# Optimization experiments

Measured on AMD Instinct MI355X. Metric: run time of the kernel, lower is better.

The kernel has to match this reference:

```python
import jax, jax.numpy as jnp
import numpy as np

TOP_K = 8
NUM_EXPERTS = 64
ALPHA = 0.01  # load_balance_alpha
TEMPERATURE = 1.0  # buffer value at init; eval mode so never decayed


def setup_inputs() -> dict:
    key = jax.random.key(0)
    k1, k2 = jax.random.split(key)
    x = jax.random.normal(k1, (4, 4096, 4096), dtype=jnp.float32)
    W_gate = jax.random.normal(k2, (64, 4096), dtype=jnp.float32) * (1.0 / np.sqrt(4096.0))
    return {"x": x, "W_gate": W_gate}


def reference(x, W_gate):
    B, S, H = x.shape
    x_flat = x.reshape(-1, H)                       # [N, H], N = B*S
    N = x_flat.shape[0]
    logits = jnp.einsum('nh,eh->ne', x_flat, W_gate)  # gate linear, bias=False
    logits = logits / TEMPERATURE                   # eval: no noise added
    scores, idx = jax.lax.top_k(logits, TOP_K)      # [N, K] values / indices
    # scatter mask -> per-expert usage counts (equivalent to scatter_(1, idx, 1).sum(0))
    current_usage = jnp.zeros((NUM_EXPERTS,), dtype=x.dtype).at[idx.reshape(-1)].add(1.0)
    expert_load = current_usage / N
    ideal_load = 1.0 / NUM_EXPERTS
    load_balance_loss = ALPHA * jnp.sum((expert_load - ideal_load) ** 2)
    scores = jax.nn.softmax(scores.astype(jnp.float32), axis=-1).astype(x.dtype)
    return scores, idx, load_balance_loss
```

## Files before the change

kernel.cpp:

```cpp
#include <hip/hip_runtime.h>
#include <math.h>

#define NTOK 16384
#define HDIM 4096
#define NEXP 64
#define SPLITS 4
#define KRANGE (HDIM / SPLITS)
#define KC 32
#define TOKTILE 128
#define XSTRIDE (TOKTILE + 4)
#define WSTRIDE (NEXP + 4)

__global__ __launch_bounds__(512, 4) void gemm_tile(const float* __restrict__ x,
                                                    const float* __restrict__ W,
                                                    float* __restrict__ partial) {
  __shared__ __align__(16) float xs[KC][XSTRIDE];
  __shared__ __align__(16) float ws[KC][WSTRIDE];
  const int tile = (int)blockIdx.x >> 2;
  const int split = (int)blockIdx.x & 3;
  const int kbase = split * KRANGE;
  const int tok0 = tile * TOKTILE;
  const int t = (int)threadIdx.x;
  const int eg = t & 15;
  const int tg = t >> 4;

  const int srow = t >> 3;
  const int sc4 = (t & 7) * 4;
  const float* xsrc0 = x + (size_t)(tok0 + srow) * HDIM + kbase + sc4;
  const float* xsrc1 = x + (size_t)(tok0 + 64 + srow) * HDIM + kbase + sc4;
  const float* wsrc = W + (size_t)srow * HDIM + kbase + sc4;

  float4 xa0 = *(const float4*)xsrc0;
  float4 xa1 = *(const float4*)xsrc1;
  float4 wa = *(const float4*)wsrc;

  double acc[4][4];
#pragma unroll
  for (int i = 0; i < 4; ++i)
#pragma unroll
    for (int j = 0; j < 4; ++j) acc[i][j] = 0.0;

  for (int c = 0; c < KRANGE / KC; ++c) {
#pragma unroll
    for (int j = 0; j < 4; ++j) {
      xs[sc4 + j][srow] = ((const float*)&xa0)[j];
      xs[sc4 + j][64 + srow] = ((const float*)&xa1)[j];
      ws[sc4 + j][srow] = ((const float*)&wa)[j];
    }
    __syncthreads();
    if (c + 1 < KRANGE / KC) {
      xa0 = *(const float4*)(xsrc0 + (c + 1) * KC);
      xa1 = *(const float4*)(xsrc1 + (c + 1) * KC);
      wa = *(const float4*)(wsrc + (c + 1) * KC);
    }
    float p[4][4];
#pragma unroll
    for (int i = 0; i < 4; ++i)
#pragma unroll
      for (int j = 0; j < 4; ++j) p[i][j] = 0.0f;

#pragma unroll 8
    for (int k = 0; k < KC; ++k) {
      float4 xv = *(const float4*)&xs[k][4 * tg];
      float4 wv = *(const float4*)&ws[k][4 * eg];
#pragma unroll
      for (int i = 0; i < 4; ++i) {
        float xi = ((const float*)&xv)[i];
        p[i][0] = fmaf(xi, wv.x, p[i][0]);
        p[i][1] = fmaf(xi, wv.y, p[i][1]);
        p[i][2] = fmaf(xi, wv.z, p[i][2]);
        p[i][3] = fmaf(xi, wv.w, p[i][3]);
      }
    }
#pragma unroll
    for (int i = 0; i < 4; ++i)
#pragma unroll
      for (int j = 0; j < 4; ++j) acc[i][j] += (double)p[i][j];
    __syncthreads();
  }

#pragma unroll
  for (int j = 0; j < 4; ++j) {
    float4 o;
    o.x = (float)acc[0][j]; o.y = (float)acc[1][j];
    o.z = (float)acc[2][j]; o.w = (float)acc[3][j];
    *(float4*)&partial[((size_t)split * NEXP + 4 * eg + j) * NTOK + tok0 + 4 * tg] = o;
  }
}

__global__ __launch_bounds__(128) void topk_kernel(const float* __restrict__ partial,
                                                   float* __restrict__ out_scores,
                                                   float* __restrict__ out_idx,
                                                   unsigned int* __restrict__ counts) {
  const int n = blockIdx.x * 128 + threadIdx.x;
  __shared__ unsigned int lcnt[64];
  if (threadIdx.x < 64) lcnt[threadIdx.x] = 0u;
  __syncthreads();

  float v[8];
  int id[8];
#pragma unroll
  for (int j = 0; j < 8; ++j) { v[j] = -INFINITY; id[j] = 0; }

  for (int e = 0; e < 64; ++e) {
    double s = 0.0;
#pragma unroll
    for (int sp = 0; sp < SPLITS; ++sp)
      s += (double)partial[((size_t)sp * NEXP + e) * NTOK + n];
    float val = (float)s;
#pragma unroll
    for (int j = 7; j >= 0; --j) {
      if (val > v[j]) {
        if (j == 0 || val <= v[j - 1]) { v[j] = val; id[j] = e; }
        else { v[j] = v[j - 1]; id[j] = id[j - 1]; }
      }
    }
  }

  float ex[8], s = 0.0f;
#pragma unroll
  for (int j = 0; j < 8; ++j) { ex[j] = expf(v[j] - v[0]); s += ex[j]; }
  float inv = 1.0f / s;

#pragma unroll
  for (int j = 0; j < 8; ++j) {
    out_scores[(size_t)n * 8 + j] = ex[j] * inv;
    out_idx[(size_t)n * 8 + j] = (float)id[j];
    atomicAdd(&lcnt[id[j]], 1u);
  }
  __syncthreads();
  if (threadIdx.x < 64) atomicAdd(&counts[threadIdx.x], lcnt[threadIdx.x]);
}

__global__ __launch_bounds__(64) void loss_kernel(const unsigned int* __restrict__ counts,
                                                  float* __restrict__ out_loss) {
  const int e = threadIdx.x;
  double d = (double)counts[e] / (double)NTOK - 1.0 / 64.0;
  double sq = d * d;
#pragma unroll
  for (int off = 32; off > 0; off >>= 1) sq += __shfl_down(sq, off);
  if (e == 0) *out_loss = (float)(0.01 * sq);
}

extern "C" void kernel_launch(void* const* d_in, const int* in_sizes, int n_in,
                              void* d_out, int out_size, void* d_ws, size_t ws_size,
                              hipStream_t stream) {
  const float* x = (const float*)d_in[0];
  const float* W = (const float*)d_in[1];

  float* out = (float*)d_out;
  float* scores = out;
  float* idxf = out + (size_t)NTOK * 8;
  float* loss = out + (size_t)NTOK * 16;

  unsigned int* counts = (unsigned int*)d_ws;
  float* partial = (float*)((char*)d_ws + 256);

  hipMemsetAsync(d_ws, 0, 256, stream);
  gemm_tile<<<(NTOK / TOKTILE) * SPLITS, 512, 0, stream>>>(x, W, partial);
  topk_kernel<<<NTOK / 128, 128, 0, stream>>>(partial, scores, idxf, counts);
  loss_kernel<<<1, 64, 0, stream>>>(counts, loss);
}
```

Baseline: 453.3 us.

## Retile gating GEMM with 8x8 register blocking, swizzled LDS, wave-parallel top-k

Reworks the gating GEMM to 256-token tiles with 8 K-splits and an 8x8 fp32 register tile per thread. It replaces the transposed padded LDS layout with an XOR-swizzled float4 layout and drops the double-precision per-chunk accumulation. The partial logits are now stored token-major, so top-k can give each token one wavefront: each lane holds one expert and the 8 maxima are found by shuffle reductions. The aim is more FMA work per LDS read and less fp64 conversion cost, at the price of slightly different rounding from pure fp32 accumulation and more workspace traffic for the 8 splits.

```diff
diff --git a/kernel.cpp b/kernel.cpp
--- a/kernel.cpp
+++ b/kernel.cpp
@@ -4,137 +4,168 @@
 #define NTOK 16384
 #define HDIM 4096
 #define NEXP 64
-#define SPLITS 4
+#define SPLITS 8
 #define KRANGE (HDIM / SPLITS)
 #define KC 32
-#define TOKTILE 128
-#define XSTRIDE (TOKTILE + 4)
-#define WSTRIDE (NEXP + 4)
+#define NCHUNK (KRANGE / KC)
+#define TOKTILE 256
 
-__global__ __launch_bounds__(512, 4) void gemm_tile(const float* __restrict__ x,
+#define XGRAN 2048
+#define WGRAN 512
+#define BUFGRAN (XGRAN + WGRAN)
+
+__global__ __launch_bounds__(256, 2) void gemm_tile(const float* __restrict__ x,
                                                     const float* __restrict__ W,
                                                     float* __restrict__ partial) {
-  __shared__ __align__(16) float xs[KC][XSTRIDE];
-  __shared__ __align__(16) float ws[KC][WSTRIDE];
-  const int tile = (int)blockIdx.x >> 2;
-  const int split = (int)blockIdx.x & 3;
+  __shared__ __align__(16) float4 lds4[BUFGRAN];
+  const int bid = (int)blockIdx.x;
+  const int tile = bid >> 3;
+  const int split = bid & 7;
+  const int tok0 = tile * TOKTILE;
   const int kbase = split * KRANGE;
-  const int tok0 = tile * TOKTILE;
   const int t = (int)threadIdx.x;
-  const int eg = t & 15;
-  const int tg = t >> 4;
+  const int tg = t >> 3;
+  const int eg = t & 7;
 
   const int srow = t >> 3;
-  const int sc4 = (t & 7) * 4;
-  const float* xsrc0 = x + (size_t)(tok0 + srow) * HDIM + kbase + sc4;
-  const float* xsrc1 = x + (size_t)(tok0 + 64 + srow) * HDIM + kbase + sc4;
-  const float* wsrc = W + (size_t)srow * HDIM + kbase + sc4;
+  const int scg = t & 7;
+  const float* xsrc[8];
+  int xdst[8];
+#pragma unroll
+  for (int s = 0; s < 8; ++s) {
+    const int row = s * 32 + srow;
+    xsrc[s] = x + (size_t)(tok0 + row) * HDIM + kbase + scg * 4;
+    xdst[s] = row * 8 + (scg ^ ((row >> 3) & 7));
+  }
+  const float* wsrc[2];
+  int wdst[2];
+#pragma unroll
+  for (int s = 0; s < 2; ++s) {
+    const int row = s * 32 + srow;
+    wsrc[s] = W + (size_t)row * HDIM + kbase + scg * 4;
+    wdst[s] = XGRAN + row * 8 + (scg ^ ((row >> 3) & 7));
+  }
 
-  float4 xa0 = *(const float4*)xsrc0;
-  float4 xa1 = *(const float4*)xsrc1;
-  float4 wa = *(const float4*)wsrc;
+  float acc[8][8];
+#pragma unroll
+  for (int i = 0; i < 8; ++i)
+#pragma unroll
+    for (int j = 0; j < 8; ++j) acc[i][j] = 0.0f;
 
-  double acc[4][4];
+  float4 xa[8], wa[2];
 #pragma unroll
-  for (int i = 0; i < 4; ++i)
+  for (int s = 0; s < 8; ++s) xa[s] = *(const float4*)xsrc[s];
 #pragma unroll
-    for (int j = 0; j < 4; ++j) acc[i][j] = 0.0;
+  for (int s = 0; s < 2; ++s) wa[s] = *(const float4*)wsrc[s];
 
-  for (int c = 0; c < KRANGE / KC; ++c) {
+  const float4* xs4 = lds4 + tg * 64;
+  const float4* ws4 = lds4 + XGRAN + eg * 64;
+  const int xsw = tg & 7;
+
+#pragma unroll 1
+  for (int c = 0; c < NCHUNK; ++c) {
+    __syncthreads();
 #pragma unroll
-    for (int j = 0; j < 4; ++j) {
-      xs[sc4 + j][srow] = ((const float*)&xa0)[j];
-      xs[sc4 + j][64 + srow] = ((const float*)&xa1)[j];
-      ws[sc4 + j][srow] = ((const float*)&wa)[j];
+    for (int s = 0; s < 8; ++s) lds4[xdst[s]] = xa[s];
+#pragma unroll
+    for (int s = 0; s < 2; ++s) lds4[wdst[s]] = wa[s];
+    __syncthreads();
+
+    if (c + 1 < NCHUNK) {
+#pragma unroll
+      for (int s = 0; s < 8; ++s) xa[s] = *(const float4*)(xsrc[s] + (c + 1) * KC);
+#pragma unroll
+      for (int s = 0; s < 2; ++s) wa[s] = *(const float4*)(wsrc[s] + (c + 1) * KC);
     }
-    __syncthreads();
-    if (c + 1 < KRANGE / KC) {
-      xa0 = *(const float4*)(xsrc0 + (c + 1) * KC);
-      xa1 = *(const float4*)(xsrc1 + (c + 1) * KC);
-      wa = *(const float4*)(wsrc + (c + 1) * KC);
+
+#pragma unroll
+    for (int k4 = 0; k4 < 8; ++k4) {
+      float4 xf[8], wf[8];
+#pragma unroll
+      for (int i = 0; i < 8; ++i) xf[i] = xs4[i * 8 + (k4 ^ xsw)];
+#pragma unroll
+      for (int j = 0; j < 8; ++j) wf[j] = ws4[j * 8 + (k4 ^ eg)];
+#pragma unroll
+      for (int i = 0; i < 8; ++i)
+#pragma unroll
+        for (int j = 0; j < 8; ++j) {
+          acc[i][j] = fmaf(xf[i].x, wf[j].x, acc[i][j]);
+          acc[i][j] = fmaf(xf[i].y, wf[j].y, acc[i][j]);
+          acc[i][j] = fmaf(xf[i].z, wf[j].z, acc[i][j]);
+          acc[i][j] = fmaf(xf[i].w, wf[j].w, acc[i][j]);
+        }
     }
-    float p[4][4];
-#pragma unroll
-    for (int i = 0; i < 4; ++i)
-#pragma unroll
-      for (int j = 0; j < 4; ++j) p[i][j] = 0.0f;
-
-#pragma unroll 8
-    for (int k = 0; k < KC; ++k) {
-      float4 xv = *(const float4*)&xs[k][4 * tg];
-      float4 wv = *(const float4*)&ws[k][4 * eg];
-#pragma unroll
-      for (int i = 0; i < 4; ++i) {
-        float xi = ((const float*)&xv)[i];
-        p[i][0] = fmaf(xi, wv.x, p[i][0]);
-        p[i][1] = fmaf(xi, wv.y, p[i][1]);
-        p[i][2] = fmaf(xi, wv.z, p[i][2]);
-        p[i][3] = fmaf(xi, wv.w, p[i][3]);
-      }
-    }
-#pragma unroll
-    for (int i = 0; i < 4; ++i)
-#pragma unroll
-      for (int j = 0; j < 4; ++j) acc[i][j] += (double)p[i][j];
-    __syncthreads();
   }
 
 #pragma unroll
-  for (int j = 0; j < 4; ++j) {
-    float4 o;
-    o.x = (float)acc[0][j]; o.y = (float)acc[1][j];
-    o.z = (float)acc[2][j]; o.w = (float)acc[3][j];
-    *(float4*)&partial[((size_t)split * NEXP + 4 * eg + j) * NTOK + tok0 + 4 * tg] = o;
+  for (int i = 0; i < 8; ++i) {
+    const int tok = tok0 + tg * 8 + i;
+    float* dst = partial + ((size_t)split * NTOK + tok) * NEXP + eg * 8;
+    float4 o0 = {acc[i][0], acc[i][1], acc[i][2], acc[i][3]};
+    float4 o1 = {acc[i][4], acc[i][5], acc[i][6], acc[i][7]};
+    *(float4*)dst = o0;
+    *(float4*)(dst + 4) = o1;
   }
 }
 
-__global__ __launch_bounds__(128) void topk_kernel(const float* __restrict__ partial,
+__global__ __launch_bounds__(256) void topk_kernel(const float* __restrict__ partial,
                                                    float* __restrict__ out_scores,
                                                    float* __restrict__ out_idx,
                                                    unsigned int* __restrict__ counts) {
-  const int n = blockIdx.x * 128 + threadIdx.x;
   __shared__ unsigned int lcnt[64];
-  if (threadIdx.x < 64) lcnt[threadIdx.x] = 0u;
+  const int t = (int)threadIdx.x;
+  if (t < 64) lcnt[t] = 0u;
   __syncthreads();
 
-  float v[8];
-  int id[8];
+  const int n = (int)blockIdx.x * 4 + (t >> 6);
+  const int lane = t & 63;
+
+  float lg = 0.0f;
 #pragma unroll
-  for (int j = 0; j < 8; ++j) { v[j] = -INFINITY; id[j] = 0; }
+  for (int sp = 0; sp < SPLITS; ++sp)
+    lg += partial[((size_t)sp * NTOK + n) * NEXP + lane];
 
-  for (int e = 0; e < 64; ++e) {
-    double s = 0.0;
+  float v = lg;
+  const int vi = lane;
+  float sv[8];
+  int si[8];
 #pragma unroll
-    for (int sp = 0; sp < SPLITS; ++sp)
-      s += (double)partial[((size_t)sp * NEXP + e) * NTOK + n];
-    float val = (float)s;
+  for (int j = 0; j < 8; ++j) {
+    float bv = v;
+    int bi = vi;
 #pragma unroll
-    for (int j = 7; j >= 0; --j) {
-      if (val > v[j]) {
-        if (j == 0 || val <= v[j - 1]) { v[j] = val; id[j] = e; }
-        else { v[j] = v[j - 1]; id[j] = id[j - 1]; }
-      }
+    for (int off = 32; off > 0; off >>= 1) {
+      float ov = __shfl_xor(bv, off);
+      int oi = __shfl_xor(bi, off);
+      if (ov > bv || (ov == bv && oi < bi)) { bv = ov; bi = oi; }
     }
+    sv[j] = bv;
+    si[j] = bi;
+    if (vi == bi) v = -INFINITY;
   }
 
-  float ex[8], s = 0.0f;
+  float ex[8], sum = 0.0f;
 #pragma unroll
-  for (int j = 0; j < 8; ++j) { ex[j] = expf(v[j] - v[0]); s += ex[j]; }
-  float inv = 1.0f / s;
+  for (int j = 0; j < 8; ++j) { ex[j] = expf(sv[j] - sv[0]); sum += ex[j]; }
+  const float inv = 1.0f / sum;
 
+  if (lane < 8) {
+    float me = ex[0];
+    int mi = si[0];
 #pragma unroll
-  for (int j = 0; j < 8; ++j) {
-    out_scores[(size_t)n * 8 + j] = ex[j] * inv;
-    out_idx[(size_t)n * 8 + j] = (float)id[j];
-    atomicAdd(&lcnt[id[j]], 1u);
+    for (int j = 1; j < 8; ++j)
+      if (lane == j) { me = ex[j]; mi = si[j]; }
+    out_scores[(size_t)n * 8 + lane] = me * inv;
+    out_idx[(size_t)n * 8 + lane] = (float)mi;
+    atomicAdd(&lcnt[mi], 1u);
   }
   __syncthreads();
-  if (threadIdx.x < 64) atomicAdd(&counts[threadIdx.x], lcnt[threadIdx.x]);
+  if (t < 64) atomicAdd(&counts[t], lcnt[t]);
 }
 
 __global__ __launch_bounds__(64) void loss_kernel(const unsigned int* __restrict__ counts,
                                                   float* __restrict__ out_loss) {
-  const int e = threadIdx.x;
+  const int e = (int)threadIdx.x;
   double d = (double)counts[e] / (double)NTOK - 1.0 / 64.0;
   double sq = d * d;
 #pragma unroll
@@ -157,7 +188,7 @@
   float* partial = (float*)((char*)d_ws + 256);
 
   hipMemsetAsync(d_ws, 0, 256, stream);
-  gemm_tile<<<(NTOK / TOKTILE) * SPLITS, 512, 0, stream>>>(x, W, partial);
-  topk_kernel<<<NTOK / 128, 128, 0, stream>>>(partial, scores, idxf, counts);
+  gemm_tile<<<(NTOK / TOKTILE) * SPLITS, 256, 0, stream>>>(x, W, partial);
+  topk_kernel<<<NTOK / 4, 256, 0, stream>>>(partial, scores, idxf, counts);
   loss_kernel<<<1, 64, 0, stream>>>(counts, loss);
 }
```

Result: slower. 675.4 us (+49.0%).
